# Kernel optimization log

Hardware: AMD Instinct MI355X
Metric: run time of the kernel (lower is better)

Reference implementation:

```python
import jax, jax.numpy as jnp
import numpy as np

STRIDE = 16.0
PRE_NMS_TOP_N = 6000
POST_NMS_TOP_N = 1000
NMS_THRESH = 0.7
MIN_SIZE = 0.0
BBOX_XFORM_CLIP = float(np.log(1000.0 / 16.0))

# ---- Detectron-style anchor generation (numpy, setup-time only) ----

def _whctrs(a):
    w = a[2] - a[0] + 1
    h = a[3] - a[1] + 1
    return w, h, a[0] + 0.5 * (w - 1), a[1] + 0.5 * (h - 1)

def _mkanchors(ws, hs, xc, yc):
    return np.stack([xc - 0.5 * (ws - 1), yc - 0.5 * (hs - 1),
                     xc + 0.5 * (ws - 1), yc + 0.5 * (hs - 1)], axis=1)

def _ratio_enum(a, ratios):
    w, h, xc, yc = _whctrs(a)
    size = w * h
    ws = np.round(np.sqrt(size / ratios))
    hs = np.round(ws * ratios)
    return _mkanchors(ws, hs, xc, yc)

def _scale_enum(a, scales):
    w, h, xc, yc = _whctrs(a)
    return _mkanchors(w * scales, h * scales, xc, yc)

def generate_anchors(stride=16.0, sizes=(32, 64, 128, 256, 512), aspect_ratios=(0.5, 1.0, 2.0)):
    scales = np.array(sizes, dtype=np.float64) / stride
    ratios = np.array(aspect_ratios, dtype=np.float64)
    base = np.array([1, 1, stride, stride], dtype=np.float64) - 1
    ra = _ratio_enum(base, ratios)
    return np.vstack([_scale_enum(ra[i], scales) for i in range(ra.shape[0])]).astype(np.float32)


def conv2d(x, w, b, pad):
    y = jax.lax.conv_general_dilated(x, w, (1, 1), [(pad, pad), (pad, pad)],
                                     dimension_numbers=('NCHW', 'OIHW', 'NCHW'))
    return y + b[None, :, None, None]


def _proposals_one(scores, deltas, iminfo, anchors):
    # scores: (A,H,W) sigmoid probs; deltas: (4A,H,W); iminfo: [im_h, im_w, im_scale]
    A, H, W = scores.shape
    gx, gy = jnp.meshgrid(jnp.arange(W, dtype=scores.dtype) * STRIDE,
                          jnp.arange(H, dtype=scores.dtype) * STRIDE)
    shifts = jnp.stack([gx, gy, gx, gy], axis=-1)  # (H,W,4)
    all_anchors = (shifts[:, :, None, :] + anchors[None, None]).reshape(-1, 4)  # (H*W*A,4)
    sc = scores.transpose(1, 2, 0).reshape(-1)      # (H*W*A,)  anchor-minor, matches Detectron
    dl = deltas.transpose(1, 2, 0).reshape(-1, 4)   # (H*W*A,4)

    top_sc, idx = jax.lax.top_k(sc, PRE_NMS_TOP_N)  # descending scores
    boxes = all_anchors[idx]
    d = dl[idx]

    # bbox_transform decode (weights = 1)
    widths = boxes[:, 2] - boxes[:, 0] + 1.0
    heights = boxes[:, 3] - boxes[:, 1] + 1.0
    ctr_x = boxes[:, 0] + 0.5 * widths
    ctr_y = boxes[:, 1] + 0.5 * heights
    dx, dy = d[:, 0], d[:, 1]
    dw = jnp.minimum(d[:, 2], BBOX_XFORM_CLIP)
    dh = jnp.minimum(d[:, 3], BBOX_XFORM_CLIP)
    pcx = dx * widths + ctr_x
    pcy = dy * heights + ctr_y
    pw = jnp.exp(dw) * widths
    ph = jnp.exp(dh) * heights
    x1 = pcx - 0.5 * pw
    y1 = pcy - 0.5 * ph
    x2 = pcx + 0.5 * pw - 1.0
    y2 = pcy + 0.5 * ph - 1.0

    im_h, im_w, im_scale = iminfo[0], iminfo[1], iminfo[2]
    x1 = jnp.clip(x1, 0.0, im_w - 1.0)
    y1 = jnp.clip(y1, 0.0, im_h - 1.0)
    x2 = jnp.clip(x2, 0.0, im_w - 1.0)
    y2 = jnp.clip(y2, 0.0, im_h - 1.0)

    ws = x2 - x1 + 1.0
    hs = y2 - y1 + 1.0
    xc = x1 + ws / 2.0
    yc = y1 + hs / 2.0
    ms = MIN_SIZE * im_scale
    valid = (ws >= ms) & (hs >= ms) & (xc < im_w) & (yc < im_h)

    boxes_s = jnp.stack([x1, y1, x2, y2], axis=1)

    # greedy NMS over score-sorted boxes (invalid boxes start suppressed)
    areas = ws * hs
    ix1 = jnp.maximum(x1[:, None], x1[None, :])
    iy1 = jnp.maximum(y1[:, None], y1[None, :])
    ix2 = jnp.minimum(x2[:, None], x2[None, :])
    iy2 = jnp.minimum(y2[:, None], y2[None, :])
    iw = jnp.maximum(ix2 - ix1 + 1.0, 0.0)
    ih = jnp.maximum(iy2 - iy1 + 1.0, 0.0)
    inter = iw * ih
    iou = inter / (areas[:, None] + areas[None, :] - inter)

    N = PRE_NMS_TOP_N
    rng = jnp.arange(N)

    def body(i, keep):
        sup = (iou[i] > NMS_THRESH) & (rng > i)
        return jnp.where(keep[i], keep & ~sup, keep)

    keep = jax.lax.fori_loop(0, N, body, valid)

    final_sc = jnp.where(keep, jnp.where(valid, top_sc, -1.0), -1.0)
    out_sc, kidx = jax.lax.top_k(final_sc, POST_NMS_TOP_N)
    out_boxes = boxes_s[kidx]
    return out_boxes, out_sc


def setup_inputs() -> dict:
    key = jax.random.key(0)
    ks = jax.random.split(key, 5)
    B, C, H, W = 2, 512, 50, 84
    A = 15  # 5 sizes x 3 aspect ratios
    x = jax.random.normal(ks[0], (B, C, H, W), jnp.float32)
    conv_w = 0.01 * jax.random.normal(ks[1], (C, C, 3, 3), jnp.float32)
    conv_b = jnp.zeros((C,), jnp.float32)
    cls_w = 0.01 * jax.random.normal(ks[2], (A, C, 1, 1), jnp.float32)
    cls_b = jnp.zeros((A,), jnp.float32)
    bbox_w = 0.01 * jax.random.normal(ks[3], (4 * A, C, 1, 1), jnp.float32)
    bbox_b = jnp.zeros((4 * A,), jnp.float32)
    anchors = jnp.asarray(generate_anchors(STRIDE))
    im_info = jnp.array([[800.0, 1333.0, 1.6], [800.0, 1333.0, 1.6]], jnp.float32)
    return {'x': x, 'im_info': im_info, 'conv_w': conv_w, 'conv_b': conv_b,
            'cls_w': cls_w, 'cls_b': cls_b, 'bbox_w': bbox_w, 'bbox_b': bbox_b,
            'anchors': anchors}


def reference(x, im_info, conv_w, conv_b, cls_w, cls_b, bbox_w, bbox_b, anchors):
    h = jax.nn.relu(conv2d(x, conv_w, conv_b, 1))
    rpn_cls_logits = conv2d(h, cls_w, cls_b, 0)        # (B, A, H, W)
    rpn_bbox_pred = conv2d(h, bbox_w, bbox_b, 0)       # (B, 4A, H, W)
    rpn_cls_prob = jax.nn.sigmoid(rpn_cls_logits)      # CLS_ACTIVATION = 'sigmoid'
    boxes, probs = jax.vmap(_proposals_one, in_axes=(0, 0, 0, None))(
        rpn_cls_prob, rpn_bbox_pred, im_info, anchors)  # (B, POST_NMS, 4), (B, POST_NMS)
    B = x.shape[0]
    bidx = jnp.broadcast_to(jnp.arange(B, dtype=boxes.dtype)[:, None, None],
                            (B, POST_NMS_TOP_N, 1))
    rpn_rois = jnp.concatenate([bidx, boxes], axis=-1)  # (B, POST_NMS, 5)
    return rpn_cls_logits, rpn_bbox_pred, rpn_rois, probs
```

## Files before the change

kernel.cpp:

```cpp
#include <hip/hip_runtime.h>
#include <cstdint>
#include <cstddef>

typedef unsigned long long u64;
typedef unsigned int u32;

constexpr int B_ = 2, C_ = 512, H_ = 50, W_ = 84, A_ = 15;
constexpr int HW_ = H_ * W_;
constexpr int NS_ = HW_ * A_;
constexpr int PRE_ = 6000, POST_ = 1000;
constexpr int WORDS_ = 94;
constexpr int NPAD_ = 6016;
constexpr int SORTN_ = 8192;
constexpr double NMS_T = 0.7;
constexpr double CLIP_ = 4.1351665567423556;
constexpr int OUT_ROIS_ = B_ * A_ * HW_ + B_ * 4 * A_ * HW_;
constexpr int OUT_PROBS_ = OUT_ROIS_ + B_ * POST_ * 5;

__global__ void k_wt(const float* __restrict__ w, double* __restrict__ wt64) {
  int idx = blockIdx.x * 256 + threadIdx.x;
  if (idx >= C_ * C_ * 9) return;
  int co = idx & 511;
  int r = idx >> 9;
  int k = r % 9;
  int ci = r / 9;
  wt64[idx] = (double)w[(co * C_ + ci) * 9 + k];
}

__global__ void k_hzero(double* __restrict__ h0, double* __restrict__ h1) {
  size_t i = (size_t)blockIdx.x * 256 + threadIdx.x;
  if (i < (size_t)B_ * C_ * HW_) { h0[i] = 0.0; h1[i] = 0.0; }
}

__global__ __launch_bounds__(256) void k_conv3(const float* __restrict__ x,
                                               const double* __restrict__ wt64,
                                               double* __restrict__ h0,
                                               double* __restrict__ h1) {
  const int tid = threadIdx.x;
  const int lane = tid & 63;
  const int wid = __builtin_amdgcn_readfirstlane(tid >> 6);
  const int cg = lane % 12;
  const int rowg = lane / 12;
  const bool act = (rowg < 5);
  const int colb = blockIdx.x;
  const int rowb = blockIdx.y;
  const int z = blockIdx.z;
  const int b = z >> 6;
  const int cob = (z >> 2) & 15;
  const int q = z & 3;
  const int c0 = colb * 12;
  const int rblk = rowb * 10;
  const int col = c0 + cg;
  const int rg5 = act ? rowg : 4;
  const int r0 = rblk + rg5 * 2;
  const int cstart = q * 32;
  double* __restrict__ hp = (q < 2) ? h0 : h1;

  __shared__ double xs[4][14][14];

  double acc[2][8];
#pragma unroll
  for (int j = 0; j < 2; ++j)
#pragma unroll
    for (int c = 0; c < 8; ++c) acc[j][c] = 0.0;

  float xreg[3];
  auto loadX = [&](int cb4) {
#pragma unroll
    for (int k = 0; k < 3; ++k) {
      int s = tid + k * 256;
      float v = 0.f;
      if (s < 672) {
        int ci = s / 168;
        int r168 = s % 168;
        int rr = r168 / 14;
        int cc = r168 % 14;
        int gr = rblk - 1 + rr, gc = c0 - 1 + cc;
        if (gr >= 0 && gr < H_ && gc >= 0 && gc < W_)
          v = x[((b * C_ + cb4 * 4 + ci) * H_ + gr) * W_ + gc];
      }
      xreg[k] = v;
    }
  };
  auto storeX = [&]() {
#pragma unroll
    for (int k = 0; k < 3; ++k) {
      int s = tid + k * 256;
      if (s < 672) {
        int ci = s / 168;
        int r168 = s % 168;
        int rr = r168 / 14;
        int cc = r168 % 14;
        xs[ci][cc][rr] = (double)xreg[k];
      }
    }
  };

  const double* __restrict__ wb = wt64 + (size_t)(cob * 32 + wid * 8);

  loadX(cstart);
  for (int it = 0; it < 32; ++it) {
    const int cb4 = cstart + it;
    __syncthreads();
    storeX();
    __syncthreads();
    if (it < 31) loadX(cb4 + 1);
#pragma unroll
    for (int ci = 0; ci < 4; ++ci) {
#pragma unroll
      for (int kx = 0; kx < 3; ++kx) {
        double xv[4];
        const double* xp = &xs[ci][cg + kx][rg5 * 2];
#pragma unroll
        for (int t = 0; t < 4; ++t) xv[t] = xp[t];
#pragma unroll
        for (int ky = 0; ky < 3; ++ky) {
          const double* __restrict__ wp =
              wb + ((size_t)(cb4 * 4 + ci) * 9 + (ky * 3 + kx)) * C_;
#pragma unroll
          for (int c = 0; c < 8; ++c) {
            double wv = wp[c];
            acc[0][c] = fma(xv[ky], wv, acc[0][c]);
            acc[1][c] = fma(xv[ky + 1], wv, acc[1][c]);
          }
        }
      }
    }
  }

  if (act) {
#pragma unroll
    for (int c = 0; c < 8; ++c) {
      int co = cob * 32 + wid * 8 + c;
#pragma unroll
      for (int j = 0; j < 2; ++j) {
        atomicAdd(&hp[((size_t)b * C_ + co) * HW_ + (r0 + j) * W_ + col], acc[j][c]);
      }
    }
  }
}

__global__ __launch_bounds__(256) void k_conv1(const double* __restrict__ h0,
                                               const double* __restrict__ h1,
                                               const float* __restrict__ convb,
                                               const float* __restrict__ clsw,
                                               const float* __restrict__ clsb,
                                               const float* __restrict__ bbw,
                                               const float* __restrict__ bbb,
                                               float* __restrict__ out,
                                               double* __restrict__ scores,
                                               double* __restrict__ deltas) {
  const int b = blockIdx.y;
  const int p0 = blockIdx.x * 32;
  const int tid = threadIdx.x;
  const int px = tid & 31, cg = tid >> 5;
  __shared__ double hs[64][32];
  __shared__ double wl[64][80];
  double acc[10];
#pragma unroll
  for (int k = 0; k < 10; ++k) acc[k] = 0.0;
  for (int ci0 = 0; ci0 < C_; ci0 += 64) {
    for (int s = tid; s < 64 * 32; s += 256) {
      int ci = s >> 5, pp = s & 31;
      int p = p0 + pp;
      double v = 0.0;
      if (p < HW_) {
        size_t idx = ((size_t)b * C_ + ci0 + ci) * HW_ + p;
        v = (h0[idx] + h1[idx]) + (double)convb[ci0 + ci];
        v = v > 0.0 ? v : 0.0;
      }
      hs[ci][pp] = v;
    }
    for (int s = tid; s < 64 * 80; s += 256) {
      int ci = s / 80, c = s % 80;
      double v = 0.0;
      if (c < 15) v = (double)clsw[c * C_ + ci0 + ci];
      else if (c < 75) v = (double)bbw[(c - 15) * C_ + ci0 + ci];
      wl[ci][c] = v;
    }
    __syncthreads();
    for (int ci = 0; ci < 64; ++ci) {
      double xv = hs[ci][px];
#pragma unroll
      for (int k = 0; k < 10; ++k)
        acc[k] = fma(wl[ci][cg * 10 + k], xv, acc[k]);
    }
    __syncthreads();
  }
  int p = p0 + px;
  if (p < HW_) {
#pragma unroll
    for (int k = 0; k < 10; ++k) {
      int c = cg * 10 + k;
      if (c < 15) {
        double z = acc[k] + (double)clsb[c];
        out[(size_t)b * NS_ + c * HW_ + p] = (float)z;
        double s = 1.0 / (1.0 + exp(-z));
        scores[(size_t)b * NS_ + (size_t)p * A_ + c] = s;
      } else if (c < 75) {
        int cbx = c - 15;
        double z = acc[k] + (double)bbb[cbx];
        out[(size_t)B_ * NS_ + (size_t)b * (4 * A_ * HW_) + cbx * HW_ + p] = (float)z;
        deltas[(size_t)b * (4 * NS_) + (size_t)p * (4 * A_) + cbx] = z;
      }
    }
  }
}

__global__ void k_selzero(u64* __restrict__ selprefix, u32* __restrict__ selabove,
                          u32* __restrict__ selcnt, u32* __restrict__ selhist) {
  int t = blockIdx.x * 256 + threadIdx.x;
  if (t < 2) { selprefix[t] = 0ull; selabove[t] = 0u; selcnt[t] = 0u; }
  if (t < 512) selhist[t] = 0u;
}

__global__ void k_fill(u64* __restrict__ selk, u32* __restrict__ seli) {
  int b = blockIdx.y;
  int i = blockIdx.x * 256 + threadIdx.x;
  if (i < SORTN_) {
    selk[(size_t)b * SORTN_ + i] = 0ull;
    seli[(size_t)b * SORTN_ + i] = 0xFFFFFFFFu;
  }
}

__global__ __launch_bounds__(256) void k_hist(const double* __restrict__ scores,
                                              const u64* __restrict__ selprefix,
                                              u32* __restrict__ selhist, int r) {
  const int b = blockIdx.y;
  const double* sc = scores + (size_t)b * NS_;
  const int lane = (int)(threadIdx.x & 63);
  const int shift = 56 - 8 * r;
  const u64 prefix = selprefix[b];
  const u64 himask = (r == 0) ? 0ull : (~0ull << (shift + 8));
  for (int i = blockIdx.x * 256 + (int)threadIdx.x; i < NS_; i += 64 * 256) {
    u64 k = (u64)__double_as_longlong(sc[i]);
    bool valid = ((k & himask) == (prefix & himask));
    u32 d = (u32)((k >> shift) & 255);
    u64 m = __ballot(valid);
#pragma unroll
    for (int bit = 0; bit < 8; ++bit) {
      u64 bb = __ballot((d >> bit) & 1);
      m &= ((d >> bit) & 1) ? bb : ~bb;
    }
    if (valid && lane == (__ffsll((unsigned long long)m) - 1))
      atomicAdd(&selhist[b * 256 + (int)d], (u32)__popcll(m));
  }
}

__global__ void k_pick(u64* __restrict__ selprefix, u32* __restrict__ selabove,
                       u32* __restrict__ selhist, int r) {
  const int b = blockIdx.x;
  __shared__ u32 hsm[256];
  hsm[threadIdx.x] = selhist[b * 256 + threadIdx.x];
  __syncthreads();
  if (threadIdx.x == 0) {
    const int shift = 56 - 8 * r;
    u32 c = selabove[b];
    int dsel = 0;
    for (int dd = 255; dd >= 0; --dd) {
      u32 nc = c + hsm[dd];
      if (nc >= (u32)PRE_) { dsel = dd; break; }
      c = nc;
    }
    selprefix[b] |= ((u64)dsel << shift);
    selabove[b] = c;
  }
  __syncthreads();
  selhist[b * 256 + threadIdx.x] = 0u;
}

__global__ __launch_bounds__(256) void k_compact(const double* __restrict__ scores,
                                                 const u64* __restrict__ selprefix,
                                                 u32* __restrict__ selcnt,
                                                 u64* __restrict__ selk,
                                                 u32* __restrict__ seli) {
  const int b = blockIdx.y;
  const double* sc = scores + (size_t)b * NS_;
  const int lane = (int)(threadIdx.x & 63);
  const u64 T = selprefix[b];
  for (int i = blockIdx.x * 256 + (int)threadIdx.x; i < NS_; i += 64 * 256) {
    u64 k = (u64)__double_as_longlong(sc[i]);
    bool q = (k >= T);
    u64 bal = __ballot(q);
    if (bal) {
      int leader = __ffsll((unsigned long long)bal) - 1;
      u32 wbase = 0;
      if (lane == leader) wbase = atomicAdd(&selcnt[b], (u32)__popcll(bal));
      wbase = (u32)__shfl((int)wbase, leader);
      if (q) {
        u64 below = (lane == 0) ? 0ull : (~0ull >> (64 - lane));
        u32 pos = wbase + (u32)__popcll(bal & below);
        if (pos < (u32)SORTN_) {
          selk[(size_t)b * SORTN_ + pos] = k;
          seli[(size_t)b * SORTN_ + pos] = (u32)i;
        }
      }
    }
  }
}

__global__ __launch_bounds__(1024) void k_sort(const u64* __restrict__ selk,
                                               const u32* __restrict__ seli,
                                               double* __restrict__ ssc,
                                               u32* __restrict__ sidx) {
  const int b = blockIdx.x;
  __shared__ u64 kk[SORTN_];
  __shared__ u32 vv[SORTN_];
  for (int i = threadIdx.x; i < SORTN_; i += 1024) {
    kk[i] = selk[(size_t)b * SORTN_ + i];
    vv[i] = seli[(size_t)b * SORTN_ + i];
  }
  __syncthreads();
  for (int k = 2; k <= SORTN_; k <<= 1) {
    for (int j = k >> 1; j > 0; j >>= 1) {
      for (int t = threadIdx.x; t < SORTN_; t += 1024) {
        int ixj = t ^ j;
        if (ixj > t) {
          u64 ka = kk[t], kb2 = kk[ixj];
          u32 va = vv[t], vb = vv[ixj];
          bool aBetter = (ka > kb2) || (ka == kb2 && va < vb);
          bool bBetter = (kb2 > ka) || (kb2 == ka && vb < va);
          bool up = (t & k) == 0;
          bool sw = up ? bBetter : aBetter;
          if (sw) {
            kk[t] = kb2; kk[ixj] = ka;
            vv[t] = vb;  vv[ixj] = va;
          }
        }
      }
      __syncthreads();
    }
  }
  for (int i = threadIdx.x; i < PRE_; i += 1024) {
    ssc[(size_t)b * PRE_ + i] = __longlong_as_double((long long)kk[i]);
    sidx[(size_t)b * PRE_ + i] = vv[i];
  }
}

__global__ __launch_bounds__(256) void k_decode(const u32* __restrict__ sidx,
                                                const double* __restrict__ deltas,
                                                const float* __restrict__ anchors,
                                                const float* __restrict__ iminfo,
                                                double* __restrict__ boxes,
                                                double* __restrict__ areas,
                                                u64* __restrict__ vmask) {
#pragma clang fp contract(off)
  const int b = blockIdx.y;
  const int i = blockIdx.x * 256 + (int)threadIdx.x;
  bool valid = false;
  if (i < NPAD_) {
    double x1 = 0, y1 = 0, x2 = 0, y2 = 0, ar = 0;
    if (i < PRE_) {
      u32 idx = sidx[(size_t)b * PRE_ + i];
      int p = (int)idx / A_, a = (int)idx % A_;
      int yy = p / W_, xx = p % W_;
      double sx = xx * 16.0, sy = yy * 16.0;
      double b0 = sx + (double)anchors[a * 4 + 0];
      double b1 = sy + (double)anchors[a * 4 + 1];
      double b2 = sx + (double)anchors[a * 4 + 2];
      double b3 = sy + (double)anchors[a * 4 + 3];
      double wdt = b2 - b0 + 1.0, hgt = b3 - b1 + 1.0;
      double cx = b0 + 0.5 * wdt, cy = b1 + 0.5 * hgt;
      const double* d = deltas + (size_t)b * (4 * NS_) + (size_t)idx * 4;
      double dx = d[0], dy = d[1];
      double dw = d[2] < CLIP_ ? d[2] : CLIP_;
      double dh = d[3] < CLIP_ ? d[3] : CLIP_;
      double pcx = dx * wdt + cx, pcy = dy * hgt + cy;
      double pw = exp(dw) * wdt, ph = exp(dh) * hgt;
      x1 = pcx - 0.5 * pw;
      y1 = pcy - 0.5 * ph;
      x2 = pcx + 0.5 * pw - 1.0;
      y2 = pcy + 0.5 * ph - 1.0;
      double imh = (double)iminfo[b * 3 + 0];
      double imw = (double)iminfo[b * 3 + 1];
      x1 = x1 < 0.0 ? 0.0 : (x1 > imw - 1.0 ? imw - 1.0 : x1);
      y1 = y1 < 0.0 ? 0.0 : (y1 > imh - 1.0 ? imh - 1.0 : y1);
      x2 = x2 < 0.0 ? 0.0 : (x2 > imw - 1.0 ? imw - 1.0 : x2);
      y2 = y2 < 0.0 ? 0.0 : (y2 > imh - 1.0 ? imh - 1.0 : y2);
      double wss = x2 - x1 + 1.0, hss = y2 - y1 + 1.0;
      double xc = x1 + wss / 2.0, yc = y1 + hss / 2.0;
      valid = (wss >= 0.0) && (hss >= 0.0) && (xc < imw) && (yc < imh);
      ar = wss * hss;
    }
    double* bx = boxes + ((size_t)b * NPAD_ + i) * 4;
    bx[0] = x1; bx[1] = y1; bx[2] = x2; bx[3] = y2;
    areas[(size_t)b * NPAD_ + i] = ar;
  }
  u64 bal = __ballot(valid);
  if ((threadIdx.x & 63) == 0) {
    int w = i >> 6;
    if (w < WORDS_) vmask[b * WORDS_ + w] = bal;
  }
}

__global__ __launch_bounds__(64) void k_mask(const double* __restrict__ boxes,
                                             const double* __restrict__ areas,
                                             u64* __restrict__ mask) {
#pragma clang fp contract(off)
  const int b = blockIdx.z;
  const int wc = blockIdx.x, rb = blockIdx.y;
  const int i = rb * 64 + (int)threadIdx.x;
  if (wc < rb) {
    if (i < PRE_) mask[((size_t)b * NPAD_ + i) * WORDS_ + wc] = 0ull;
    return;
  }
  __shared__ double cbx[64][4];
  __shared__ double car[64];
  {
    int sj = wc * 64 + (int)threadIdx.x;
    const double* pj = boxes + ((size_t)b * NPAD_ + sj) * 4;
    cbx[threadIdx.x][0] = pj[0];
    cbx[threadIdx.x][1] = pj[1];
    cbx[threadIdx.x][2] = pj[2];
    cbx[threadIdx.x][3] = pj[3];
    car[threadIdx.x] = areas[(size_t)b * NPAD_ + sj];
  }
  __syncthreads();
  if (i >= PRE_) return;
  const double* bi = boxes + ((size_t)b * NPAD_ + i) * 4;
  double x1 = bi[0], y1 = bi[1], x2 = bi[2], y2 = bi[3];
  double ai = areas[(size_t)b * NPAD_ + i];
  u64 m = 0;
  int jmax = PRE_ - wc * 64;
  if (jmax > 64) jmax = 64;
  for (int j2 = 0; j2 < jmax; ++j2) {
    int j = wc * 64 + j2;
    if (j > i) {
      double ix1 = x1 > cbx[j2][0] ? x1 : cbx[j2][0];
      double iy1 = y1 > cbx[j2][1] ? y1 : cbx[j2][1];
      double ix2 = x2 < cbx[j2][2] ? x2 : cbx[j2][2];
      double iy2 = y2 < cbx[j2][3] ? y2 : cbx[j2][3];
      double iw = ix2 - ix1 + 1.0;
      if (iw < 0.0) iw = 0.0;
      double ih = iy2 - iy1 + 1.0;
      if (ih < 0.0) ih = 0.0;
      double inter = iw * ih;
      double iou = inter / (ai + car[j2] - inter);
      if (iou > NMS_T) m |= (1ull << j2);
    }
  }
  mask[((size_t)b * NPAD_ + i) * WORDS_ + wc] = m;
}

__global__ __launch_bounds__(64) void k_scan(const u64* __restrict__ mask,
                                             const u64* __restrict__ vmask,
                                             u64* __restrict__ keepm) {
  const int b = blockIdx.x;
  const int lane = (int)threadIdx.x;
  u64 rem0 = ~vmask[b * WORDS_ + lane];
  u64 rem1 = (lane < WORDS_ - 64) ? ~vmask[b * WORDS_ + 64 + lane] : ~0ull;
  int kept = 0;
  int Bb = 0;
  for (; Bb < WORDS_ && kept < POST_; ++Bb) {
    const int base = Bb * 64;
    int lim = PRE_ - base;
    if (lim > 64) lim = 64;
    u64 cur = (Bb < 64) ? __shfl(rem0, Bb) : __shfl(rem1, Bb - 64);
    if (lim < 64) cur |= (~0ull) << lim;
    u64 dg = (lane < lim) ? mask[((size_t)b * NPAD_ + base + lane) * WORDS_ + Bb] : 0ull;
    u64 kb = 0;
    while (cur != ~0ull) {
      int t = __ffsll((unsigned long long)~cur) - 1;
      kb |= 1ull << t;
      cur |= __shfl(dg, t);
      cur |= 1ull << t;
      if (++kept >= POST_) break;
    }
    u64 or0 = 0, or1 = 0;
    u64 k2 = kb;
    const u64* mb = mask + (size_t)b * NPAD_ * WORDS_;
    while (k2) {
      int t0 = __ffsll((unsigned long long)k2) - 1; k2 &= k2 - 1;
      int t1 = -1, t2 = -1, t3 = -1;
      if (k2) { t1 = __ffsll((unsigned long long)k2) - 1; k2 &= k2 - 1; }
      if (k2) { t2 = __ffsll((unsigned long long)k2) - 1; k2 &= k2 - 1; }
      if (k2) { t3 = __ffsll((unsigned long long)k2) - 1; k2 &= k2 - 1; }
      const u64* m0 = mb + (size_t)(base + t0) * WORDS_;
      u64 a0 = m0[lane];
      u64 a1 = (lane < WORDS_ - 64) ? m0[64 + lane] : 0ull;
      u64 b0 = 0, b1 = 0, c0 = 0, c1 = 0, d0 = 0, d1 = 0;
      if (t1 >= 0) {
        const u64* m1 = mb + (size_t)(base + t1) * WORDS_;
        b0 = m1[lane]; b1 = (lane < WORDS_ - 64) ? m1[64 + lane] : 0ull;
      }
      if (t2 >= 0) {
        const u64* m2 = mb + (size_t)(base + t2) * WORDS_;
        c0 = m2[lane]; c1 = (lane < WORDS_ - 64) ? m2[64 + lane] : 0ull;
      }
      if (t3 >= 0) {
        const u64* m3 = mb + (size_t)(base + t3) * WORDS_;
        d0 = m3[lane]; d1 = (lane < WORDS_ - 64) ? m3[64 + lane] : 0ull;
      }
      or0 |= (a0 | b0) | (c0 | d0);
      or1 |= (a1 | b1) | (c1 | d1);
    }
    rem0 |= or0;
    rem1 |= or1;
    if (lane == 0) keepm[b * WORDS_ + Bb] = kb;
  }
  for (int w = Bb + lane; w < WORDS_; w += 64)
    keepm[b * WORDS_ + w] = 0ull;
}

__global__ __launch_bounds__(256) void k_final(const u64* __restrict__ keepm,
                                               const double* __restrict__ boxes,
                                               const double* __restrict__ ssc,
                                               float* __restrict__ out) {
  const int b = blockIdx.x;
  __shared__ u32 pk[WORDS_ + 1];
  __shared__ u64 km_s[WORDS_];
  for (int w = threadIdx.x; w < WORDS_; w += 256) km_s[w] = keepm[b * WORDS_ + w];
  __syncthreads();
  if (threadIdx.x == 0) {
    u32 a = 0;
    for (int w = 0; w < WORDS_; ++w) {
      pk[w] = a;
      a += (u32)__popcll(km_s[w]);
    }
    pk[WORDS_] = a;
  }
  __syncthreads();
  const u32 K = pk[WORDS_];
  for (int i = threadIdx.x; i < PRE_; i += 256) {
    int w = i >> 6, t = i & 63;
    u64 km = km_s[w];
    u32 before = pk[w] + (u32)__popcll(km & ((1ull << t) - 1ull));
    bool kp = (km >> t) & 1ull;
    int slot = kp ? (int)before : (int)K + (i - (int)before);
    if (slot < POST_) {
      const double* bx = boxes + ((size_t)b * NPAD_ + i) * 4;
      float* ro = out + OUT_ROIS_ + ((size_t)b * POST_ + slot) * 5;
      ro[0] = (float)b;
      ro[1] = (float)bx[0];
      ro[2] = (float)bx[1];
      ro[3] = (float)bx[2];
      ro[4] = (float)bx[3];
      out[OUT_PROBS_ + b * POST_ + slot] = kp ? (float)ssc[(size_t)b * PRE_ + i] : -1.0f;
    }
  }
}

extern "C" void kernel_launch(void* const* d_in, const int* in_sizes, int n_in,
                              void* d_out, int out_size, void* d_ws, size_t ws_size,
                              hipStream_t stream) {
  (void)in_sizes; (void)n_in; (void)out_size; (void)ws_size;
  const float* x = (const float*)d_in[0];
  const float* iminfo = (const float*)d_in[1];
  const float* convw = (const float*)d_in[2];
  const float* convb = (const float*)d_in[3];
  const float* clsw = (const float*)d_in[4];
  const float* clsb = (const float*)d_in[5];
  const float* bbw = (const float*)d_in[6];
  const float* bbb = (const float*)d_in[7];
  const float* anchors = (const float*)d_in[8];
  float* out = (float*)d_out;

  char* ws = (char*)d_ws;
  size_t off = 0;
  auto alloc = [&](size_t bytes) -> void* {
    void* p = ws + off;
    off += (bytes + 255) & ~(size_t)255;
    return p;
  };
  double* wt64 = (double*)alloc((size_t)C_ * 9 * C_ * 8);
  double* h0 = (double*)alloc((size_t)B_ * C_ * HW_ * 8);
  double* h1 = (double*)alloc((size_t)B_ * C_ * HW_ * 8);
  double* scores = (double*)alloc((size_t)B_ * NS_ * 8);
  double* deltas = (double*)alloc((size_t)B_ * NS_ * 4 * 8);
  u64* selk = (u64*)alloc((size_t)B_ * SORTN_ * 8);
  u32* seli = (u32*)alloc((size_t)B_ * SORTN_ * 4);
  double* ssc = (double*)alloc((size_t)B_ * PRE_ * 8);
  u32* sidx = (u32*)alloc((size_t)B_ * PRE_ * 4);
  double* boxes = (double*)alloc((size_t)B_ * NPAD_ * 4 * 8);
  double* areas = (double*)alloc((size_t)B_ * NPAD_ * 8);
  u64* vmask = (u64*)alloc((size_t)B_ * WORDS_ * 8);
  u64* mask = (u64*)alloc((size_t)B_ * NPAD_ * WORDS_ * 8);
  u64* keepm = (u64*)alloc((size_t)B_ * WORDS_ * 8);
  u64* selprefix = (u64*)alloc(2 * 8);
  u32* selabove = (u32*)alloc(2 * 4);
  u32* selcnt = (u32*)alloc(2 * 4);
  u32* selhist = (u32*)alloc(512 * 4);

  k_wt<<<(C_ * C_ * 9 + 255) / 256, 256, 0, stream>>>(convw, wt64);
  k_hzero<<<(B_ * C_ * HW_ + 255) / 256, 256, 0, stream>>>(h0, h1);
  k_conv3<<<dim3(7, 5, 128), 256, 0, stream>>>(x, wt64, h0, h1);
  k_conv1<<<dim3(132, 2), 256, 0, stream>>>(h0, h1, convb, clsw, clsb, bbw, bbb, out, scores, deltas);
  k_selzero<<<2, 256, 0, stream>>>(selprefix, selabove, selcnt, selhist);
  k_fill<<<dim3(32, 2), 256, 0, stream>>>(selk, seli);
  for (int r = 0; r < 5; ++r) {
    k_hist<<<dim3(64, 2), 256, 0, stream>>>(scores, selprefix, selhist, r);
    k_pick<<<2, 256, 0, stream>>>(selprefix, selabove, selhist, r);
  }
  k_compact<<<dim3(64, 2), 256, 0, stream>>>(scores, selprefix, selcnt, selk, seli);
  k_sort<<<2, 1024, 0, stream>>>(selk, seli, ssc, sidx);
  k_decode<<<dim3(24, 2), 256, 0, stream>>>(sidx, deltas, anchors, iminfo, boxes, areas, vmask);
  k_mask<<<dim3(94, 94, 2), 64, 0, stream>>>(boxes, areas, mask);
  k_scan<<<2, 64, 0, stream>>>(mask, vmask, keepm);
  k_final<<<2, 256, 0, stream>>>(keepm, boxes, ssc, out);
}
```

Measured before the change: 1.475 ms.

## Replace bitonic sort with parallel rank selection and shrink conv3 blocks

The single-block-per-image bitonic sort of 8192 keys is replaced by a rank kernel in which each selected element counts how many candidates beat it and scatters itself to that position, spread over 8 blocks per image. The padding fill kernel is dropped because only the live count is read. Separately, the 3x3 conv now uses 128-thread blocks covering 16 output channels, doubling the grid. Rank counting is O(n^2) compares, and the smaller conv blocks reload the input tile more often per output channel.

Result: slower. 1.999 ms (+35.5%).

```diff
diff --git a/kernel.cpp b/kernel.cpp
--- a/kernel.cpp
+++ b/kernel.cpp
@@ -32,7 +32,7 @@
   if (i < (size_t)B_ * C_ * HW_) { h0[i] = 0.0; h1[i] = 0.0; }
 }
 
-__global__ __launch_bounds__(256) void k_conv3(const float* __restrict__ x,
+__global__ __launch_bounds__(128) void k_conv3(const float* __restrict__ x,
                                                const double* __restrict__ wt64,
                                                double* __restrict__ h0,
                                                double* __restrict__ h1) {
@@ -45,8 +45,8 @@
   const int colb = blockIdx.x;
   const int rowb = blockIdx.y;
   const int z = blockIdx.z;
-  const int b = z >> 6;
-  const int cob = (z >> 2) & 15;
+  const int b = z >> 7;
+  const int cob = (z >> 2) & 31;
   const int q = z & 3;
   const int c0 = colb * 12;
   const int rblk = rowb * 10;
@@ -64,11 +64,11 @@
 #pragma unroll
     for (int c = 0; c < 8; ++c) acc[j][c] = 0.0;
 
-  float xreg[3];
+  float xreg[6];
   auto loadX = [&](int cb4) {
 #pragma unroll
-    for (int k = 0; k < 3; ++k) {
-      int s = tid + k * 256;
+    for (int k = 0; k < 6; ++k) {
+      int s = tid + k * 128;
       float v = 0.f;
       if (s < 672) {
         int ci = s / 168;
@@ -84,8 +84,8 @@
   };
   auto storeX = [&]() {
 #pragma unroll
-    for (int k = 0; k < 3; ++k) {
-      int s = tid + k * 256;
+    for (int k = 0; k < 6; ++k) {
+      int s = tid + k * 128;
       if (s < 672) {
         int ci = s / 168;
         int r168 = s % 168;
@@ -96,7 +96,7 @@
     }
   };
 
-  const double* __restrict__ wb = wt64 + (size_t)(cob * 32 + wid * 8);
+  const double* __restrict__ wb = wt64 + (size_t)(cob * 16 + wid * 8);
 
   loadX(cstart);
   for (int it = 0; it < 32; ++it) {
@@ -131,7 +131,7 @@
   if (act) {
 #pragma unroll
     for (int c = 0; c < 8; ++c) {
-      int co = cob * 32 + wid * 8 + c;
+      int co = cob * 16 + wid * 8 + c;
 #pragma unroll
       for (int j = 0; j < 2; ++j) {
         atomicAdd(&hp[((size_t)b * C_ + co) * HW_ + (r0 + j) * W_ + col], acc[j][c]);
@@ -212,15 +212,6 @@
   int t = blockIdx.x * 256 + threadIdx.x;
   if (t < 2) { selprefix[t] = 0ull; selabove[t] = 0u; selcnt[t] = 0u; }
   if (t < 512) selhist[t] = 0u;
-}
-
-__global__ void k_fill(u64* __restrict__ selk, u32* __restrict__ seli) {
-  int b = blockIdx.y;
-  int i = blockIdx.x * 256 + threadIdx.x;
-  if (i < SORTN_) {
-    selk[(size_t)b * SORTN_ + i] = 0ull;
-    seli[(size_t)b * SORTN_ + i] = 0xFFFFFFFFu;
-  }
 }
 
 __global__ __launch_bounds__(256) void k_hist(const double* __restrict__ scores,
@@ -299,41 +290,45 @@
   }
 }
 
-__global__ __launch_bounds__(1024) void k_sort(const u64* __restrict__ selk,
+__global__ __launch_bounds__(1024) void k_rank(const u64* __restrict__ selk,
                                                const u32* __restrict__ seli,
+                                               const u32* __restrict__ selcnt,
                                                double* __restrict__ ssc,
                                                u32* __restrict__ sidx) {
-  const int b = blockIdx.x;
-  __shared__ u64 kk[SORTN_];
-  __shared__ u32 vv[SORTN_];
-  for (int i = threadIdx.x; i < SORTN_; i += 1024) {
-    kk[i] = selk[(size_t)b * SORTN_ + i];
-    vv[i] = seli[(size_t)b * SORTN_ + i];
-  }
-  __syncthreads();
-  for (int k = 2; k <= SORTN_; k <<= 1) {
-    for (int j = k >> 1; j > 0; j >>= 1) {
-      for (int t = threadIdx.x; t < SORTN_; t += 1024) {
-        int ixj = t ^ j;
-        if (ixj > t) {
-          u64 ka = kk[t], kb2 = kk[ixj];
-          u32 va = vv[t], vb = vv[ixj];
-          bool aBetter = (ka > kb2) || (ka == kb2 && va < vb);
-          bool bBetter = (kb2 > ka) || (kb2 == ka && vb < va);
-          bool up = (t & k) == 0;
-          bool sw = up ? bBetter : aBetter;
-          if (sw) {
-            kk[t] = kb2; kk[ixj] = ka;
-            vv[t] = vb;  vv[ixj] = va;
-          }
-        }
-      }
-      __syncthreads();
-    }
-  }
-  for (int i = threadIdx.x; i < PRE_; i += 1024) {
-    ssc[(size_t)b * PRE_ + i] = __longlong_as_double((long long)kk[i]);
-    sidx[(size_t)b * PRE_ + i] = vv[i];
+  const int b = blockIdx.y;
+  const int e = blockIdx.x * 1024 + (int)threadIdx.x;
+  int mn = (int)selcnt[b];
+  if (mn > SORTN_) mn = SORTN_;
+  const bool active = (e < mn);
+  u64 ke = 0; u32 ie = 0;
+  if (active) {
+    ke = selk[(size_t)b * SORTN_ + e];
+    ie = seli[(size_t)b * SORTN_ + e];
+  }
+  __shared__ u64 ks[1024];
+  __shared__ u32 isx[1024];
+  int rank = 0;
+  for (int t0 = 0; t0 < mn; t0 += 1024) {
+    int j = t0 + (int)threadIdx.x;
+    if (j < mn) {
+      ks[threadIdx.x] = selk[(size_t)b * SORTN_ + j];
+      isx[threadIdx.x] = seli[(size_t)b * SORTN_ + j];
+    }
+    __syncthreads();
+    int lim = mn - t0;
+    if (lim > 1024) lim = 1024;
+    if (active) {
+      for (int j2 = 0; j2 < lim; ++j2) {
+        u64 kj = ks[j2];
+        bool better = (kj > ke) || (kj == ke && isx[j2] < ie);
+        rank += better ? 1 : 0;
+      }
+    }
+    __syncthreads();
+  }
+  if (active && rank < PRE_) {
+    ssc[(size_t)b * PRE_ + rank] = __longlong_as_double((long long)ke);
+    sidx[(size_t)b * PRE_ + rank] = ie;
   }
 }
 
@@ -583,16 +578,15 @@
 
   k_wt<<<(C_ * C_ * 9 + 255) / 256, 256, 0, stream>>>(convw, wt64);
   k_hzero<<<(B_ * C_ * HW_ + 255) / 256, 256, 0, stream>>>(h0, h1);
-  k_conv3<<<dim3(7, 5, 128), 256, 0, stream>>>(x, wt64, h0, h1);
+  k_conv3<<<dim3(7, 5, 256), 128, 0, stream>>>(x, wt64, h0, h1);
   k_conv1<<<dim3(132, 2), 256, 0, stream>>>(h0, h1, convb, clsw, clsb, bbw, bbb, out, scores, deltas);
   k_selzero<<<2, 256, 0, stream>>>(selprefix, selabove, selcnt, selhist);
-  k_fill<<<dim3(32, 2), 256, 0, stream>>>(selk, seli);
   for (int r = 0; r < 5; ++r) {
     k_hist<<<dim3(64, 2), 256, 0, stream>>>(scores, selprefix, selhist, r);
     k_pick<<<2, 256, 0, stream>>>(selprefix, selabove, selhist, r);
   }
   k_compact<<<dim3(64, 2), 256, 0, stream>>>(scores, selprefix, selcnt, selk, seli);
-  k_sort<<<2, 1024, 0, stream>>>(selk, seli, ssc, sidx);
+  k_rank<<<dim3(8, 2), 1024, 0, stream>>>(selk, seli, selcnt, ssc, sidx);
   k_decode<<<dim3(24, 2), 256, 0, stream>>>(sidx, deltas, anchors, iminfo, boxes, areas, vmask);
   k_mask<<<dim3(94, 94, 2), 64, 0, stream>>>(boxes, areas, mask);
   k_scan<<<2, 64, 0, stream>>>(mask, vmask, keepm);
```
